# Optimization experiments

Hardware: AMD Instinct MI355X
Metric: run time of the kernel (lower is better)

## Reference

```python
import jax, jax.numpy as jnp
import numpy as np

KSIZE = 3
STRIDE = 1
PAD = (KSIZE - 1) // 2
SIGMA_SPACE = 0.15 * KSIZE + 0.35  # 0.8 (module default when sigmaSpace is None)
SIGMA_COLOR = SIGMA_SPACE          # module default when sigmaColor is None


def _gaussian_kernel(ksize, sigma):
    # matches getGaussianKernel in the torch source
    center = ksize // 2
    xs = np.arange(ksize, dtype=np.float32) - center
    k1 = np.exp(-xs ** 2 / (2.0 * sigma ** 2))
    k2 = np.outer(k1, k1)
    return jnp.asarray(k2 / k2.sum(), dtype=jnp.float32)  # [k, k]


def setup_inputs() -> dict:
    key = jax.random.key(0)
    batch_img = jax.random.uniform(key, (8, 3, 512, 512), dtype=jnp.float32)
    return {"batch_img": batch_img}


def reference(batch_img):
    B, C, H, W = batch_img.shape
    # reflect pad, then extract k*k shifted views (fixed small loop over 9 offsets)
    xp = jnp.pad(batch_img, ((0, 0), (0, 0), (PAD, PAD), (PAD, PAD)), mode='reflect')
    Ho = (H + 2 * PAD - KSIZE) // STRIDE + 1
    Wo = (W + 2 * PAD - KSIZE) // STRIDE + 1
    patches = jnp.stack(
        [xp[:, :, i:i + Ho * STRIDE:STRIDE, j:j + Wo * STRIDE:STRIDE]
         for i in range(KSIZE) for j in range(KSIZE)],
        axis=-1,
    ).reshape(B, C, Ho, Wo, KSIZE, KSIZE)  # [B,C,Ho,Wo,k,k]

    center = batch_img[:, :, ::STRIDE, ::STRIDE][..., None, None]  # [B,C,Ho,Wo,1,1]
    diff_color = patches - center
    weights_color = jnp.exp(-diff_color ** 2 / (2.0 * SIGMA_COLOR ** 2))
    weights_color = weights_color / weights_color.sum(axis=(-1, -2), keepdims=True)

    weights_space = _gaussian_kernel(KSIZE, SIGMA_SPACE)  # [k,k], broadcasts
    weights = weights_space * weights_color
    weights_sum = weights.sum(axis=(-1, -2))
    weighted_pix = (weights * patches).sum(axis=(-1, -2)) / weights_sum
    return weighted_pix  # [B,C,Ho,Wo]
```

## Files before the change

kernel.cpp:

```cpp
#include <hip/hip_runtime.h>

#define HW 512

typedef float vfloat4 __attribute__((ext_vector_type(4)));

__global__ __launch_bounds__(256) void bilateral3x3(const float* __restrict__ in,
                                                    float* __restrict__ out,
                                                    int nthreads) {
    int gid = blockIdx.x * 256 + threadIdx.x;
    if (gid >= nthreads) return;

    int xg    = gid & 63;
    int yg    = (gid >> 6) & 255;
    int plane = gid >> 14;

    const float* p = in + (size_t)plane * (HW * HW);
    int x0 = xg << 3;
    int y0 = yg << 1;

    int ym = (y0 == 0)   ? 1   : y0 - 1;
    int yb = (y0 == 510) ? 510 : y0 + 2;
    int xl = (x0 == 0)   ? 1   : x0 - 1;
    int xr = (x0 == 504) ? 510 : x0 + 8;

    float A[10], B[10], C[10];
    auto loadrow = [&](float* w, int r) {
        const float* rp = p + (size_t)r * HW;
        vfloat4 a = *reinterpret_cast<const vfloat4*>(rp + x0);
        vfloat4 b = *reinterpret_cast<const vfloat4*>(rp + x0 + 4);
        w[0] = rp[xl];
        w[1] = a.x; w[2] = a.y; w[3] = a.z; w[4] = a.w;
        w[5] = b.x; w[6] = b.y; w[7] = b.z; w[8] = b.w;
        w[9] = rp[xr];
    };

    const float nC = -1.1271055f;

    auto dorow = [&](const float* T, const float* M, const float* Bo, float* op) {
        float res[8];
        #pragma unroll
        for (int j = 0; j < 8; ++j) {
            float c = M[j + 1];
            float num = c;
            float den = 1.0f;
            #pragma unroll
            for (int dx = 0; dx < 3; ++dx) {
                float spd = (float)(1 + (dx - 1) * (dx - 1));
                {
                    float pv = T[j + dx];
                    float d  = pv - c;
                    float w  = __builtin_amdgcn_exp2f(fmaf(d, d, spd) * nC);
                    num = fmaf(w, pv, num); den += w;
                }
                {
                    float pv = Bo[j + dx];
                    float d  = pv - c;
                    float w  = __builtin_amdgcn_exp2f(fmaf(d, d, spd) * nC);
                    num = fmaf(w, pv, num); den += w;
                }
                if (dx != 1) {
                    float pv = M[j + dx];
                    float d  = pv - c;
                    float w  = __builtin_amdgcn_exp2f(fmaf(d, d, 1.0f) * nC);
                    num = fmaf(w, pv, num); den += w;
                }
            }
            res[j] = num * __builtin_amdgcn_rcpf(den);
        }
        vfloat4 o0 = {res[0], res[1], res[2], res[3]};
        vfloat4 o1 = {res[4], res[5], res[6], res[7]};
        __builtin_nontemporal_store(o0, reinterpret_cast<vfloat4*>(op));
        __builtin_nontemporal_store(o1, reinterpret_cast<vfloat4*>(op) + 1);
    };

    float* outp = out + (size_t)plane * (HW * HW) + (size_t)y0 * HW + x0;

    loadrow(A, ym);
    loadrow(B, y0);
    loadrow(C, y0 + 1);
    dorow(A, B, C, outp);
    loadrow(A, yb);
    dorow(B, C, A, outp + HW);
}

extern "C" void kernel_launch(void* const* d_in, const int* in_sizes, int n_in,
                              void* d_out, int out_size, void* d_ws, size_t ws_size,
                              hipStream_t stream) {
    const float* in = (const float*)d_in[0];
    float* out = (float*)d_out;
    int total = in_sizes[0];
    int nthreads = total >> 4;
    int blocks = (nthreads + 255) / 256;
    bilateral3x3<<<blocks, 256, 0, stream>>>(in, out, nthreads);
}
```

Measured before the change: 79.57 us.

## Map one wavefront per full row band and share halo pixels via lane shuffles

Each 64-lane wavefront now covers an entire 512-wide row, and each thread produces 4 output rows instead of 2, with a rolling three-row register window. Left and right halo pixels come from neighbouring lanes through shuffles instead of extra scalar global loads, and reflect padding at the image edges is handled per lane. This cuts redundant row loads (6 rows read per 4 output rows instead of 4 per 2) and removes the halo loads. The cost is fewer threads in flight and a longer serial chain per thread.

```diff
diff --git a/kernel.cpp b/kernel.cpp
--- a/kernel.cpp
+++ b/kernel.cpp
@@ -6,32 +6,29 @@
 
 __global__ __launch_bounds__(256) void bilateral3x3(const float* __restrict__ in,
                                                     float* __restrict__ out,
-                                                    int nthreads) {
-    int gid = blockIdx.x * 256 + threadIdx.x;
-    if (gid >= nthreads) return;
+                                                    int nwaves) {
+    int wid  = blockIdx.x * 4 + ((int)threadIdx.x >> 6);
+    int lane = (int)threadIdx.x & 63;
+    if (wid >= nwaves) return;
 
-    int xg    = gid & 63;
-    int yg    = (gid >> 6) & 255;
-    int plane = gid >> 14;
+    int rg    = wid & 127;
+    int plane = wid >> 7;
+    int r0    = rg << 2;
+    int x0    = lane << 3;
 
     const float* p = in + (size_t)plane * (HW * HW);
-    int x0 = xg << 3;
-    int y0 = yg << 1;
 
-    int ym = (y0 == 0)   ? 1   : y0 - 1;
-    int yb = (y0 == 510) ? 510 : y0 + 2;
-    int xl = (x0 == 0)   ? 1   : x0 - 1;
-    int xr = (x0 == 504) ? 510 : x0 + 8;
-
-    float A[10], B[10], C[10];
+    float R0[10], R1[10], R2[10];
     auto loadrow = [&](float* w, int r) {
-        const float* rp = p + (size_t)r * HW;
-        vfloat4 a = *reinterpret_cast<const vfloat4*>(rp + x0);
-        vfloat4 b = *reinterpret_cast<const vfloat4*>(rp + x0 + 4);
-        w[0] = rp[xl];
+        const float* rp = p + (size_t)r * HW + x0;
+        vfloat4 a = *reinterpret_cast<const vfloat4*>(rp);
+        vfloat4 b = *reinterpret_cast<const vfloat4*>(rp + 4);
+        float lh = __shfl_up(b.w, 1);
+        float rh = __shfl_down(a.x, 1);
+        w[0] = (lane == 0)  ? a.y : lh;
+        w[9] = (lane == 63) ? b.z : rh;
         w[1] = a.x; w[2] = a.y; w[3] = a.z; w[4] = a.w;
         w[5] = b.x; w[6] = b.y; w[7] = b.z; w[8] = b.w;
-        w[9] = rp[xr];
     };
 
     const float nC = -1.1271055f;
@@ -73,14 +70,21 @@
         __builtin_nontemporal_store(o1, reinterpret_cast<vfloat4*>(op) + 1);
     };
 
-    float* outp = out + (size_t)plane * (HW * HW) + (size_t)y0 * HW + x0;
+    int ym = (r0 == 0)   ? 1   : r0 - 1;
+    int yb = (r0 == 508) ? 510 : r0 + 4;
 
-    loadrow(A, ym);
-    loadrow(B, y0);
-    loadrow(C, y0 + 1);
-    dorow(A, B, C, outp);
-    loadrow(A, yb);
-    dorow(B, C, A, outp + HW);
+    float* op = out + (size_t)plane * (HW * HW) + (size_t)r0 * HW + x0;
+
+    loadrow(R0, ym);
+    loadrow(R1, r0);
+    loadrow(R2, r0 + 1);
+    dorow(R0, R1, R2, op);
+    loadrow(R0, r0 + 2);
+    dorow(R1, R2, R0, op + HW);
+    loadrow(R1, r0 + 3);
+    dorow(R2, R0, R1, op + 2 * HW);
+    loadrow(R2, yb);
+    dorow(R0, R1, R2, op + 3 * HW);
 }
 
 extern "C" void kernel_launch(void* const* d_in, const int* in_sizes, int n_in,
@@ -89,7 +93,7 @@
     const float* in = (const float*)d_in[0];
     float* out = (float*)d_out;
     int total = in_sizes[0];
-    int nthreads = total >> 4;
-    int blocks = (nthreads + 255) / 256;
-    bilateral3x3<<<blocks, 256, 0, stream>>>(in, out, nthreads);
+    int nwaves = total >> 11;
+    int blocks = (nwaves + 3) / 4;
+    bilateral3x3<<<blocks, 256, 0, stream>>>(in, out, nwaves);
 }
```

Result: no change. 80.17 us (+0.8%).
